# Kernel optimization log

Hardware: AMD Instinct MI355X
Metric: run time of the kernel (lower is better)

The kernel has to match this reference:

```python
import jax, jax.numpy as jnp
import numpy as np

NC = 64
B, H, W = 32, 128, 128


def setup_inputs() -> dict:
    key = jax.random.key(0)
    kx, = jax.random.split(key, 1)
    x = jax.random.normal(kx, (B, NC, H, W), dtype=jnp.float32)
    # params as initialized in the torch module
    exp_param = jnp.eye(NC, dtype=jnp.float32)[:, :, None, None]  # (nc, nc, 1, 1)
    bias = jnp.zeros((NC, 1, 1), dtype=jnp.float32)               # (nc, 1, 1)
    return {"x": x, "exp_param": exp_param, "bias": bias}


def reference(x, exp_param, bias):
    # x: (B, nc, H, W); exp_param: (nc, nc, 1, 1); bias: (nc, 1, 1)
    xr = jax.nn.relu(x) + 0.1  # strictly positive -> log is safe
    # prod_i xr[b,i,h,w] ** E[i,j]  ==  exp( sum_i E[i,j] * log xr[b,i,h,w] )
    # Fused form avoids materializing the (B, nc, nc, H, W) intermediate.
    E = exp_param[:, :, 0, 0]  # (nc_in=i, nc_out=j)
    logx = jnp.log(xr)
    out = jnp.exp(jnp.einsum('bihw,ij->bjhw', logx, E)) + bias  # (B, nc, H, W)
    return out
```

## Files before the change

### kernel.cpp

```cpp
#include <hip/hip_runtime.h>

#define NCH 64
#define HWSZ 16384
#define NPOINTS (32 * HWSZ)
#define NTILES (NPOINTS / 64)
#define NBLOCKS 1024

typedef __attribute__((ext_vector_type(8))) short bf16x8;
typedef __attribute__((ext_vector_type(4))) float f32x4;

static __device__ __forceinline__ unsigned short bf16_trunc(float f) {
    return (unsigned short)(__float_as_uint(f) >> 16);
}
static __device__ __forceinline__ float bf16_up(unsigned short h) {
    return __uint_as_float((unsigned)h << 16);
}

__global__ __launch_bounds__(256, 2) void fused_log_einsum_exp(
    const float* __restrict__ x,
    const float* __restrict__ E,
    const float* __restrict__ bias,
    float* __restrict__ out)
{
    const int lane = threadIdx.x & 63;
    const int wv   = threadIdx.x >> 6;
    const int lg   = lane >> 4;
    const int ln   = lane & 15;

    bf16x8 ah[4][2], al[4][2];
    #pragma unroll
    for (int m = 0; m < 4; ++m) {
        #pragma unroll
        for (int kk = 0; kk < 2; ++kk) {
            bf16x8 h, l;
            #pragma unroll
            for (int e = 0; e < 8; ++e) {
                const int i = kk * 32 + lg * 8 + e;
                const int j = m * 16 + ln;
                const float v = E[i * NCH + j];
                const unsigned short hh = bf16_trunc(v);
                h[e] = (short)hh;
                l[e] = (short)bf16_trunc(v - bf16_up(hh));
            }
            ah[m][kk] = h; al[m][kk] = l;
        }
    }

    float bv[4][4];
    #pragma unroll
    for (int m = 0; m < 4; ++m)
        #pragma unroll
        for (int r = 0; r < 4; ++r)
            bv[m][r] = bias[m * 16 + lg * 4 + r];

    for (int t = blockIdx.x; t < NTILES; t += NBLOCKS) {
        const int p0 = t * 64 + wv * 16;
        const size_t base = (size_t)(p0 & ~(HWSZ - 1)) * NCH
                          + (size_t)(p0 & (HWSZ - 1)) + ln;

        float xr[2][8];
        #pragma unroll
        for (int kk = 0; kk < 2; ++kk)
            #pragma unroll
            for (int e = 0; e < 8; ++e)
                xr[kk][e] = x[base + (size_t)(kk * 32 + lg * 8 + e) * HWSZ];

        bf16x8 bh[2], bl[2];
        #pragma unroll
        for (int kk = 0; kk < 2; ++kk) {
            bf16x8 h, l;
            #pragma unroll
            for (int e = 0; e < 8; ++e) {
                const float lx = __logf(fmaxf(xr[kk][e], 0.0f) + 0.1f);
                const unsigned short hh = bf16_trunc(lx);
                h[e] = (short)hh;
                l[e] = (short)bf16_trunc(lx - bf16_up(hh));
            }
            bh[kk] = h; bl[kk] = l;
        }

        #pragma unroll
        for (int m = 0; m < 4; ++m) {
            f32x4 acc = {0.f, 0.f, 0.f, 0.f};
            #pragma unroll
            for (int kk = 0; kk < 2; ++kk) {
                acc = __builtin_amdgcn_mfma_f32_16x16x32_bf16(ah[m][kk], bh[kk], acc, 0, 0, 0);
                acc = __builtin_amdgcn_mfma_f32_16x16x32_bf16(ah[m][kk], bl[kk], acc, 0, 0, 0);
                acc = __builtin_amdgcn_mfma_f32_16x16x32_bf16(al[m][kk], bh[kk], acc, 0, 0, 0);
            }
            #pragma unroll
            for (int r = 0; r < 4; ++r) {
                const int j = m * 16 + lg * 4 + r;
                out[base + (size_t)j * HWSZ] = __expf(acc[r]) + bv[m][r];
            }
        }
    }
}

extern "C" void kernel_launch(void* const* d_in, const int* in_sizes, int n_in,
                              void* d_out, int out_size, void* d_ws, size_t ws_size,
                              hipStream_t stream) {
    const float* x    = (const float*)d_in[0];
    const float* E    = (const float*)d_in[1];
    const float* bias = (const float*)d_in[2];
    float* out = (float*)d_out;

    dim3 grid(NBLOCKS), block(256);
    hipLaunchKernelGGL(fused_log_einsum_exp, grid, block, 0, stream,
                       x, E, bias, out);
}
```

Baseline: 244.4 us.

## Double-buffer x tile loads across a fully unrolled tile loop

Replaces the grid-stride tile loop with a fully unrolled loop over 8 tiles per block. Each next tile's x values are prefetched into a second register buffer while the current tile is computed, so global-load latency overlaps the log/MFMA/exp work. It also packs the bf16 hi/lo split two values per 32-bit word with bit masks instead of per-element short inserts, and raises the occupancy hint to 3 blocks per SM. The risks are extra register pressure from the second buffer and the higher occupancy target, which could cause spills, and the hardcoded count of 8 tiles per block depends on NTILES/NBLOCKS.

```diff
diff --git a/kernel.cpp b/kernel.cpp
--- a/kernel.cpp
+++ b/kernel.cpp
@@ -9,14 +9,16 @@
 typedef __attribute__((ext_vector_type(8))) short bf16x8;
 typedef __attribute__((ext_vector_type(4))) float f32x4;
 
-static __device__ __forceinline__ unsigned short bf16_trunc(float f) {
-    return (unsigned short)(__float_as_uint(f) >> 16);
+union fragU { bf16x8 v; unsigned int u[4]; };
+
+static __device__ __forceinline__ unsigned int fbits(float f) {
+    return __float_as_uint(f);
 }
-static __device__ __forceinline__ float bf16_up(unsigned short h) {
-    return __uint_as_float((unsigned)h << 16);
+static __device__ __forceinline__ float bf16_up_bits(unsigned int b) {
+    return __uint_as_float(b & 0xFFFF0000u);
 }
 
-__global__ __launch_bounds__(256, 2) void fused_log_einsum_exp(
+__global__ __launch_bounds__(256, 3) void fused_log_einsum_exp(
     const float* __restrict__ x,
     const float* __restrict__ E,
     const float* __restrict__ bias,
@@ -32,17 +34,19 @@
     for (int m = 0; m < 4; ++m) {
         #pragma unroll
         for (int kk = 0; kk < 2; ++kk) {
-            bf16x8 h, l;
+            fragU h, l;
             #pragma unroll
-            for (int e = 0; e < 8; ++e) {
-                const int i = kk * 32 + lg * 8 + e;
-                const int j = m * 16 + ln;
-                const float v = E[i * NCH + j];
-                const unsigned short hh = bf16_trunc(v);
-                h[e] = (short)hh;
-                l[e] = (short)bf16_trunc(v - bf16_up(hh));
+            for (int w = 0; w < 4; ++w) {
+                const int i0 = kk * 32 + lg * 8 + 2 * w;
+                const int j  = m * 16 + ln;
+                const float f0 = E[i0 * NCH + j];
+                const float f1 = E[(i0 + 1) * NCH + j];
+                h.u[w] = (fbits(f1) & 0xFFFF0000u) | (fbits(f0) >> 16);
+                const float g0 = f0 - bf16_up_bits(fbits(f0));
+                const float g1 = f1 - bf16_up_bits(fbits(f1));
+                l.u[w] = (fbits(g1) & 0xFFFF0000u) | (fbits(g0) >> 16);
             }
-            ah[m][kk] = h; al[m][kk] = l;
+            ah[m][kk] = h.v; al[m][kk] = l.v;
         }
     }
 
@@ -53,32 +57,34 @@
         for (int r = 0; r < 4; ++r)
             bv[m][r] = bias[m * 16 + lg * 4 + r];
 
-    for (int t = blockIdx.x; t < NTILES; t += NBLOCKS) {
+    auto tile_base = [&](int t) -> size_t {
         const int p0 = t * 64 + wv * 16;
-        const size_t base = (size_t)(p0 & ~(HWSZ - 1)) * NCH
-                          + (size_t)(p0 & (HWSZ - 1)) + ln;
+        return (size_t)(p0 & ~(HWSZ - 1)) * NCH
+             + (size_t)(p0 & (HWSZ - 1)) + ln;
+    };
 
-        float xr[2][8];
+    auto load_tile = [&](float (&xr)[16], size_t base) {
         #pragma unroll
-        for (int kk = 0; kk < 2; ++kk)
-            #pragma unroll
-            for (int e = 0; e < 8; ++e)
-                xr[kk][e] = x[base + (size_t)(kk * 32 + lg * 8 + e) * HWSZ];
+        for (int e = 0; e < 16; ++e)
+            xr[e] = x[base + (size_t)((e >> 3) * 32 + lg * 8 + (e & 7)) * HWSZ];
+    };
 
+    auto compute_tile = [&](const float (&xr)[16], size_t base) {
         bf16x8 bh[2], bl[2];
         #pragma unroll
         for (int kk = 0; kk < 2; ++kk) {
-            bf16x8 h, l;
+            fragU h, l;
             #pragma unroll
-            for (int e = 0; e < 8; ++e) {
-                const float lx = __logf(fmaxf(xr[kk][e], 0.0f) + 0.1f);
-                const unsigned short hh = bf16_trunc(lx);
-                h[e] = (short)hh;
-                l[e] = (short)bf16_trunc(lx - bf16_up(hh));
+            for (int w = 0; w < 4; ++w) {
+                const float lx0 = __logf(fmaxf(xr[kk * 8 + 2 * w],     0.0f) + 0.1f);
+                const float lx1 = __logf(fmaxf(xr[kk * 8 + 2 * w + 1], 0.0f) + 0.1f);
+                h.u[w] = (fbits(lx1) & 0xFFFF0000u) | (fbits(lx0) >> 16);
+                const float lo0 = lx0 - bf16_up_bits(fbits(lx0));
+                const float lo1 = lx1 - bf16_up_bits(fbits(lx1));
+                l.u[w] = (fbits(lo1) & 0xFFFF0000u) | (fbits(lo0) >> 16);
             }
-            bh[kk] = h; bl[kk] = l;
+            bh[kk] = h.v; bl[kk] = l.v;
         }
-
         #pragma unroll
         for (int m = 0; m < 4; ++m) {
             f32x4 acc = {0.f, 0.f, 0.f, 0.f};
@@ -94,6 +100,23 @@
                 out[base + (size_t)j * HWSZ] = __expf(acc[r]) + bv[m][r];
             }
         }
+    };
+
+    float xA[16], xB[16];
+    size_t baseA = tile_base(blockIdx.x);
+    size_t baseB;
+    load_tile(xA, baseA);
+
+    #pragma unroll
+    for (int k = 0; k < 4; ++k) {
+        baseB = tile_base(blockIdx.x + (2 * k + 1) * NBLOCKS);
+        load_tile(xB, baseB);
+        compute_tile(xA, baseA);
+        if (k < 3) {
+            baseA = tile_base(blockIdx.x + (2 * k + 2) * NBLOCKS);
+            load_tile(xA, baseA);
+        }
+        compute_tile(xB, baseB);
     }
 }
 
```

Measured after the change: 416.1 us. 70.3% more time.
